# Performance work log

Measured on AMD Instinct MI355X. Metric: run time of the kernel, lower is better.

## Reference

```python
import jax, jax.numpy as jnp
import numpy as np
import math

D_POLY = 2  # polynomial order d
N_NODES = 50000
IN_FEATS = 128
H_FEATS = 64
N_EDGES = 800000


def calc_thetas(d):
    # Beta-wavelet polynomial coefficients (ascending order), matching calculate_theta2
    thetas = []
    for i in range(d + 1):
        p = np.poly1d([1.0])
        for _ in range(i):
            p = p * np.poly1d([0.5, 0.0])      # (x/2)
        for _ in range(d - i):
            p = p * np.poly1d([-0.5, 1.0])     # (1 - x/2)
        beta = math.gamma(i + 1) * math.gamma(d + 1 - i) / math.gamma(d + 2)
        p = p / beta
        asc = p.coeffs[::-1]                   # ascending coefficients
        asc = np.concatenate([asc, np.zeros(d + 1 - len(asc))])
        thetas.append(asc.astype(np.float32))
    return thetas

THETAS = calc_thetas(D_POLY)


def setup_inputs() -> dict:
    key = jax.random.key(0)
    ks = jax.random.split(key, 7)
    features = jax.random.normal(ks[0], (N_NODES, IN_FEATS), dtype=jnp.float32)
    src = jax.random.randint(ks[1], (N_EDGES,), 0, N_NODES)
    dst = jax.random.randint(ks[2], (N_EDGES,), 0, N_NODES)
    s1 = 1.0 / math.sqrt(IN_FEATS)
    W1 = jax.random.uniform(ks[3], (H_FEATS, IN_FEATS), jnp.float32, -s1, s1)
    b1 = jnp.zeros((H_FEATS,), jnp.float32)
    s2 = 1.0 / math.sqrt(H_FEATS * (D_POLY + 1))
    W2 = jax.random.uniform(ks[4], (H_FEATS, H_FEATS * (D_POLY + 1)), jnp.float32, -s2, s2)
    b2 = jnp.zeros((H_FEATS,), jnp.float32)
    return {"features": features, "src": src, "dst": dst,
            "W1": W1, "b1": b1, "W2": W2, "b2": b2}


def reference(features, src, dst, W1, b1, W2, b2):
    N = features.shape[0]
    # linear1 + ReLU
    x = jax.nn.relu(features @ W1.T + b1)  # [N, H]
    # D^{-1/2} from in-degrees (clamped at 1)
    deg = jax.ops.segment_sum(jnp.ones_like(dst, dtype=x.dtype), dst, num_segments=N)
    D_invsqrt = jnp.clip(deg, 1.0, None) ** -0.5  # [N]
    D_invsqrt = D_invsqrt[:, None]

    def unn_laplacian(f):
        # f - D^{-1/2} A D^{-1/2} f   (aggregation onto destination nodes)
        agg = jax.ops.segment_sum((f * D_invsqrt)[src], dst, num_segments=N)
        return f - agg * D_invsqrt

    outs = []
    for theta in THETAS:
        f = x
        h = theta[0] * x
        for k in range(1, len(theta)):
            f = unn_laplacian(f)
            h = h + theta[k] * f
        outs.append(h)
    feats_final = jnp.concatenate(outs, axis=-1)  # [N, H*(d+1)]
    return feats_final @ W2.T + b2
```

## Files before the change

### kernel.cpp

```cpp
#include <hip/hip_runtime.h>

#define NN 50000
#define NE 800000
#define INF 128
#define HF 64
#define K2 192
#define MAXDEG 64

typedef __attribute__((ext_vector_type(8))) short short8;
typedef __attribute__((ext_vector_type(4))) float float4v;
typedef __attribute__((ext_vector_type(4))) unsigned short ushort4v;
typedef __attribute__((ext_vector_type(2))) unsigned int uint2v;

__device__ inline unsigned short f2bf(float x) {
    unsigned int u = __float_as_uint(x);
    u += 0x7FFFu + ((u >> 16) & 1u);
    return (unsigned short)(u >> 16);
}
__device__ inline float bflo(unsigned int p) { return __uint_as_float(p << 16); }
__device__ inline float bfhi(unsigned int p) { return __uint_as_float(p & 0xFFFF0000u); }


__global__ __launch_bounds__(256) void fill_ell_part(const int* __restrict__ src,
                                                     const int* __restrict__ dst,
                                                     int* __restrict__ cnt,
                                                     unsigned short* __restrict__ ell) {
    int chunk = blockIdx.x >> 3;
    int p     = blockIdx.x & 7;
    int e = chunk * 256 + threadIdx.x;
    if (e >= NE) return;
    int d = dst[e];
    if (d / 6250 != p) return;
    int pos = atomicAdd(&cnt[d], 1);
    if (pos < MAXDEG) ell[d * MAXDEG + pos] = (unsigned short)src[e];
}

__global__ __launch_bounds__(256) void dinv_kernel(int* __restrict__ cnt,
                                                   float* __restrict__ dinv,
                                                   unsigned short* __restrict__ hb0,
                                                   unsigned short* __restrict__ hb1) {
    int i = blockIdx.x * 256 + threadIdx.x;
    if (i < NN) {
        int c = cnt[i];
        if (c > MAXDEG) c = MAXDEG;
        cnt[i] = c;
        dinv[i] = rsqrtf((float)(c < 1 ? 1 : c));
    }
    if (i < HF) {
        hb0[(size_t)NN * HF + i] = 0;
        hb1[(size_t)NN * HF + i] = 0;
    }
}


__global__ void pack_b(const float* __restrict__ W1, const float* __restrict__ W2,
                       unsigned short* __restrict__ Bp1, unsigned short* __restrict__ Bp2,
                       int* __restrict__ cnt) {
    int gid = blockIdx.x * 256 + threadIdx.x;
    for (int z = gid; z < NN; z += 20480) cnt[z] = 0;
    if (gid >= 20480) return;
    if (gid < 8192) {
        int j  = gid & 7;
        int l  = (gid >> 3) & 63;
        int nt = (gid >> 9) & 3;
        int kc = gid >> 11;
        int n = nt * 16 + (l & 15);
        int k = kc * 32 + (l >> 4) * 8 + j;
        Bp1[gid] = f2bf(W1[n * INF + k]);
    } else {
        int g = gid - 8192;
        int j  = g & 7;
        int l  = (g >> 3) & 63;
        int nt = (g >> 9) & 3;
        int kc = g >> 11;
        int n = nt * 16 + (l & 15);
        int k = kc * 32 + (l >> 4) * 8 + j;
        const float* row = W2 + (size_t)n * K2;
        float v;
        if (k < 64) {
            v = 3.0f * row[k];
        } else if (k < 128) {
            int c = k - 64;
            v = -3.0f * row[c] + 3.0f * row[64 + c];
        } else {
            int c = k - 128;
            v = 0.75f * row[c] - 1.5f * row[64 + c] + 0.75f * row[128 + c];
        }
        Bp2[g] = f2bf(v);
    }
}


__global__ __launch_bounds__(256) void gemm1_mfma(const float* __restrict__ F,
                                                  const unsigned short* __restrict__ Bp,
                                                  const float* __restrict__ b1,
                                                  const float* __restrict__ dinv,
                                                  unsigned short* __restrict__ xb,
                                                  unsigned short* __restrict__ hb0) {
    int tid  = threadIdx.x;
    int lane = tid & 63;
    int wv   = tid >> 6;
    int m0   = blockIdx.x * 64 + wv * 16;
    if (m0 >= NN) return;
    int mrow = lane & 15;
    int q    = lane >> 4;

    float4v acc[4];
#pragma unroll
    for (int nt = 0; nt < 4; ++nt) acc[nt] = (float4v){0.f, 0.f, 0.f, 0.f};

    const float* arow = F + (size_t)(m0 + mrow) * INF + q * 8;
#pragma unroll
    for (int kc = 0; kc < INF / 32; ++kc) {
        const float* ap = arow + kc * 32;
        float4v a0 = *reinterpret_cast<const float4v*>(ap);
        float4v a1 = *reinterpret_cast<const float4v*>(ap + 4);
        short8 af;
        af[0] = (short)f2bf(a0[0]); af[1] = (short)f2bf(a0[1]);
        af[2] = (short)f2bf(a0[2]); af[3] = (short)f2bf(a0[3]);
        af[4] = (short)f2bf(a1[0]); af[5] = (short)f2bf(a1[1]);
        af[6] = (short)f2bf(a1[2]); af[7] = (short)f2bf(a1[3]);
#pragma unroll
        for (int nt = 0; nt < 4; ++nt) {
            short8 bf = *reinterpret_cast<const short8*>(Bp + (((kc * 4 + nt) * 64 + lane) << 3));
            acc[nt] = __builtin_amdgcn_mfma_f32_16x16x32_bf16(af, bf, acc[nt], 0, 0, 0);
        }
    }

    float dn[4];
#pragma unroll
    for (int r = 0; r < 4; ++r) dn[r] = dinv[m0 + q * 4 + r];

#pragma unroll
    for (int nt = 0; nt < 4; ++nt) {
        int n = nt * 16 + mrow;
        float bv = b1[n];
#pragma unroll
        for (int r = 0; r < 4; ++r) {
            int node = m0 + q * 4 + r;
            float v = acc[nt][r] + bv;
            v = v > 0.0f ? v : 0.0f;
            xb [(size_t)node * HF + n] = f2bf(v);
            hb0[(size_t)node * HF + n] = f2bf(v * dn[r]);
        }
    }
}


template <bool WRITE_H>
__global__ __launch_bounds__(256) void gather_quad(const unsigned short* __restrict__ ell,
                                                   const int* __restrict__ cnt,
                                                   const float* __restrict__ dinv,
                                                   const unsigned short* __restrict__ fin,
                                                   const unsigned short* __restrict__ hb,
                                                   unsigned short* __restrict__ fout,
                                                   unsigned short* __restrict__ hout) {
    int lane  = threadIdx.x & 63;
    int wv    = threadIdx.x >> 6;
    int which = lane >> 4;
    int jj    = lane & 15;
    int n = blockIdx.x * 16 + wv * 4 + which;
    int deg = cnt[n];

    ushort4v ids = *reinterpret_cast<const ushort4v*>(ell + (size_t)n * MAXDEG + jj * 4);
    int slot = jj * 4;
    int s0 = (slot + 0 < deg) ? (int)ids[0] : NN;
    int s1 = (slot + 1 < deg) ? (int)ids[1] : NN;
    int s2 = (slot + 2 < deg) ? (int)ids[2] : NN;
    int s3 = (slot + 3 < deg) ? (int)ids[3] : NN;

    int wmax = deg;
    wmax = max(wmax, __shfl_xor(wmax, 16));
    wmax = max(wmax, __shfl_xor(wmax, 32));

    const uint2v* hbd = (const uint2v*)hb;
    int base = which * 16;

    float a0=0,a1=0,a2=0,a3=0;
    float b0=0,b1=0,b2=0,b3=0;
    float c0=0,c1=0,c2=0,c3=0;
    float d0=0,d1=0,d2=0,d3=0;

    for (int k = 0; k < wmax; k += 4) {
        int o = base + (k >> 2);
        int t0 = __shfl(s0, o), t1 = __shfl(s1, o);
        int t2 = __shfl(s2, o), t3 = __shfl(s3, o);
        uint2v p0 = hbd[(size_t)t0 * 16 + jj];
        uint2v p1 = hbd[(size_t)t1 * 16 + jj];
        uint2v p2 = hbd[(size_t)t2 * 16 + jj];
        uint2v p3 = hbd[(size_t)t3 * 16 + jj];
        a0 += bflo(p0[0]); a1 += bfhi(p0[0]); a2 += bflo(p0[1]); a3 += bfhi(p0[1]);
        b0 += bflo(p1[0]); b1 += bfhi(p1[0]); b2 += bflo(p1[1]); b3 += bfhi(p1[1]);
        c0 += bflo(p2[0]); c1 += bfhi(p2[0]); c2 += bflo(p2[1]); c3 += bfhi(p2[1]);
        d0 += bflo(p3[0]); d1 += bfhi(p3[0]); d2 += bflo(p3[1]); d3 += bfhi(p3[1]);
    }
    float e0 = (a0 + b0) + (c0 + d0);
    float e1 = (a1 + b1) + (c1 + d1);
    float e2 = (a2 + b2) + (c2 + d2);
    float e3 = (a3 + b3) + (c3 + d3);
    float dn = dinv[n];

    uint2v xv = ((const uint2v*)fin)[(size_t)n * 16 + jj];
    float f0 = bflo(xv[0]) - e0 * dn;
    float f1 = bfhi(xv[0]) - e1 * dn;
    float f2 = bflo(xv[1]) - e2 * dn;
    float f3 = bfhi(xv[1]) - e3 * dn;
    uint2v ov;
    ov[0] = (unsigned int)f2bf(f0) | ((unsigned int)f2bf(f1) << 16);
    ov[1] = (unsigned int)f2bf(f2) | ((unsigned int)f2bf(f3) << 16);
    ((uint2v*)fout)[(size_t)n * 16 + jj] = ov;
    if (WRITE_H) {
        uint2v hv;
        hv[0] = (unsigned int)f2bf(f0 * dn) | ((unsigned int)f2bf(f1 * dn) << 16);
        hv[1] = (unsigned int)f2bf(f2 * dn) | ((unsigned int)f2bf(f3 * dn) << 16);
        ((uint2v*)hout)[(size_t)n * 16 + jj] = hv;
    }
}


__global__ __launch_bounds__(256) void gemm2_mfma(const unsigned short* __restrict__ xb,
                                                  const unsigned short* __restrict__ f1b,
                                                  const unsigned short* __restrict__ f2b,
                                                  const unsigned short* __restrict__ Bp,
                                                  const float* __restrict__ b2,
                                                  float* __restrict__ out) {
    int tid  = threadIdx.x;
    int lane = tid & 63;
    int wv   = tid >> 6;
    int m0   = blockIdx.x * 64 + wv * 16;
    if (m0 >= NN) return;
    int mrow = lane & 15;
    int q    = lane >> 4;

    float4v acc[4];
#pragma unroll
    for (int nt = 0; nt < 4; ++nt) acc[nt] = (float4v){0.f, 0.f, 0.f, 0.f};

    const unsigned short* ax = xb  + (size_t)(m0 + mrow) * HF + q * 8;
    const unsigned short* a1 = f1b + (size_t)(m0 + mrow) * HF + q * 8;
    const unsigned short* a2 = f2b + (size_t)(m0 + mrow) * HF + q * 8;

#pragma unroll
    for (int kc = 0; kc < 6; ++kc) {
        short8 af;
        if (kc < 2)      af = *reinterpret_cast<const short8*>(ax + kc * 32);
        else if (kc < 4) af = *reinterpret_cast<const short8*>(a1 + (kc - 2) * 32);
        else             af = *reinterpret_cast<const short8*>(a2 + (kc - 4) * 32);
#pragma unroll
        for (int nt = 0; nt < 4; ++nt) {
            short8 bf = *reinterpret_cast<const short8*>(Bp + (((kc * 4 + nt) * 64 + lane) << 3));
            acc[nt] = __builtin_amdgcn_mfma_f32_16x16x32_bf16(af, bf, acc[nt], 0, 0, 0);
        }
    }

#pragma unroll
    for (int nt = 0; nt < 4; ++nt) {
        int n = nt * 16 + mrow;
        float bv = b2[n];
#pragma unroll
        for (int r = 0; r < 4; ++r) {
            int node = m0 + q * 4 + r;
            out[(size_t)node * HF + n] = acc[nt][r] + bv;
        }
    }
}


extern "C" void kernel_launch(void* const* d_in, const int* in_sizes, int n_in,
                              void* d_out, int out_size, void* d_ws, size_t ws_size,
                              hipStream_t stream) {
    const float* features = (const float*)d_in[0];
    const int*   src      = (const int*)d_in[1];
    const int*   dst      = (const int*)d_in[2];
    const float* W1       = (const float*)d_in[3];
    const float* b1       = (const float*)d_in[4];
    const float* W2       = (const float*)d_in[5];
    const float* b2       = (const float*)d_in[6];
    float* out = (float*)d_out;

    unsigned short* xb  = (unsigned short*)d_ws;
    unsigned short* hb0 = xb  + (size_t)NN * HF;
    unsigned short* f1b = hb0 + (size_t)(NN + 1) * HF;
    unsigned short* hb1 = f1b + (size_t)NN * HF;
    unsigned short* f2b = hb1 + (size_t)(NN + 1) * HF;
    unsigned short* Bp1 = f2b + (size_t)NN * HF;
    unsigned short* Bp2 = Bp1 + 8192;
    unsigned short* ell = Bp2 + 12288;
    int*   cnt  = (int*)(ell + (size_t)NN * MAXDEG);
    float* dinv = (float*)(cnt + NN);

    pack_b<<<80, 256, 0, stream>>>(W1, W2, Bp1, Bp2, cnt);

    fill_ell_part<<<((NE + 255) / 256) * 8, 256, 0, stream>>>(src, dst, cnt, ell);

    dinv_kernel<<<(NN + 255) / 256, 256, 0, stream>>>(cnt, dinv, hb0, hb1);

    gemm1_mfma<<<(NN + 63) / 64, 256, 0, stream>>>(features, Bp1, b1, dinv, xb, hb0);

    gather_quad<true ><<<NN / 16, 256, 0, stream>>>(ell, cnt, dinv, xb,  hb0, f1b, hb1);
    gather_quad<false><<<NN / 16, 256, 0, stream>>>(ell, cnt, dinv, f1b, hb1, f2b, nullptr);

    gemm2_mfma<<<(NN + 63) / 64, 256, 0, stream>>>(xb, f1b, f2b, Bp2, b2, out);
}
```

Baseline: 170.4 us.

## Fuse second gather into GEMM2, drop dinv kernel, vectorize ELL fill

Fuses the second Laplacian gather into the output GEMM. The f2 tile is staged in shared memory instead of being written to and re-read from global memory. The dinv kernel is removed: degree clamping and rsqrt are recomputed inline from cnt, and the sentinel-row zeroing moves into pack_b. The ELL fill now loads four dst entries per thread, and the gather loop is unrolled to issue two groups of loads per iteration. The cost is lower parallelism in the fused kernel (one wave handles 16 nodes sequentially) and extra LDS use.

```diff
diff --git a/kernel.cpp b/kernel.cpp
--- a/kernel.cpp
+++ b/kernel.cpp
@@ -27,37 +27,31 @@
                                                      unsigned short* __restrict__ ell) {
     int chunk = blockIdx.x >> 3;
     int p     = blockIdx.x & 7;
-    int e = chunk * 256 + threadIdx.x;
-    if (e >= NE) return;
-    int d = dst[e];
-    if (d / 6250 != p) return;
-    int pos = atomicAdd(&cnt[d], 1);
-    if (pos < MAXDEG) ell[d * MAXDEG + pos] = (unsigned short)src[e];
-}
-
-__global__ __launch_bounds__(256) void dinv_kernel(int* __restrict__ cnt,
-                                                   float* __restrict__ dinv,
-                                                   unsigned short* __restrict__ hb0,
-                                                   unsigned short* __restrict__ hb1) {
-    int i = blockIdx.x * 256 + threadIdx.x;
-    if (i < NN) {
-        int c = cnt[i];
-        if (c > MAXDEG) c = MAXDEG;
-        cnt[i] = c;
-        dinv[i] = rsqrtf((float)(c < 1 ? 1 : c));
-    }
-    if (i < HF) {
-        hb0[(size_t)NN * HF + i] = 0;
-        hb1[(size_t)NN * HF + i] = 0;
+    int e0 = (chunk * 256 + (int)threadIdx.x) * 4;
+    if (e0 >= NE) return;
+    int4 d4 = *reinterpret_cast<const int4*>(dst + e0);
+    int dd[4] = {d4.x, d4.y, d4.z, d4.w};
+#pragma unroll
+    for (int j = 0; j < 4; ++j) {
+        int d = dd[j];
+        if (d / 6250 == p) {
+            int pos = atomicAdd(&cnt[d], 1);
+            if (pos < MAXDEG) ell[d * MAXDEG + pos] = (unsigned short)src[e0 + j];
+        }
     }
 }
 
 
 __global__ void pack_b(const float* __restrict__ W1, const float* __restrict__ W2,
                        unsigned short* __restrict__ Bp1, unsigned short* __restrict__ Bp2,
-                       int* __restrict__ cnt) {
+                       int* __restrict__ cnt,
+                       unsigned short* __restrict__ hb0, unsigned short* __restrict__ hb1) {
     int gid = blockIdx.x * 256 + threadIdx.x;
     for (int z = gid; z < NN; z += 20480) cnt[z] = 0;
+    if (gid < HF) {
+        hb0[(size_t)NN * HF + gid] = 0;
+        hb1[(size_t)NN * HF + gid] = 0;
+    }
     if (gid >= 20480) return;
     if (gid < 8192) {
         int j  = gid & 7;
@@ -94,7 +88,7 @@
 __global__ __launch_bounds__(256) void gemm1_mfma(const float* __restrict__ F,
                                                   const unsigned short* __restrict__ Bp,
                                                   const float* __restrict__ b1,
-                                                  const float* __restrict__ dinv,
+                                                  const int* __restrict__ cnt,
                                                   unsigned short* __restrict__ xb,
                                                   unsigned short* __restrict__ hb0) {
     int tid  = threadIdx.x;
@@ -129,7 +123,11 @@
 
     float dn[4];
 #pragma unroll
-    for (int r = 0; r < 4; ++r) dn[r] = dinv[m0 + q * 4 + r];
+    for (int r = 0; r < 4; ++r) {
+        int c = cnt[m0 + q * 4 + r];
+        c = c > MAXDEG ? MAXDEG : c;
+        dn[r] = rsqrtf((float)(c < 1 ? 1 : c));
+    }
 
 #pragma unroll
     for (int nt = 0; nt < 4; ++nt) {
@@ -147,10 +145,48 @@
 }
 
 
-template <bool WRITE_H>
+__device__ inline void gather_accum(const uint2v* __restrict__ hbd,
+                                    int s0, int s1, int s2, int s3,
+                                    int wmax, int base, int jj,
+                                    float& e0, float& e1, float& e2, float& e3) {
+    float a0=0,a1=0,a2=0,a3=0;
+    float b0=0,b1=0,b2=0,b3=0;
+    float c0=0,c1=0,c2=0,c3=0;
+    float d0=0,d1=0,d2=0,d3=0;
+    for (int k = 0; k < wmax; k += 8) {
+        int o = base + (k >> 2);
+        int t0 = __shfl(s0, o), t1 = __shfl(s1, o);
+        int t2 = __shfl(s2, o), t3 = __shfl(s3, o);
+        uint2v p0 = hbd[(size_t)t0 * 16 + jj];
+        uint2v p1 = hbd[(size_t)t1 * 16 + jj];
+        uint2v p2 = hbd[(size_t)t2 * 16 + jj];
+        uint2v p3 = hbd[(size_t)t3 * 16 + jj];
+        if (k + 4 < wmax) {
+            int u0 = __shfl(s0, o + 1), u1 = __shfl(s1, o + 1);
+            int u2 = __shfl(s2, o + 1), u3 = __shfl(s3, o + 1);
+            uint2v q0 = hbd[(size_t)u0 * 16 + jj];
+            uint2v q1 = hbd[(size_t)u1 * 16 + jj];
+            uint2v q2 = hbd[(size_t)u2 * 16 + jj];
+            uint2v q3 = hbd[(size_t)u3 * 16 + jj];
+            a0 += bflo(q0[0]); a1 += bfhi(q0[0]); a2 += bflo(q0[1]); a3 += bfhi(q0[1]);
+            b0 += bflo(q1[0]); b1 += bfhi(q1[0]); b2 += bflo(q1[1]); b3 += bfhi(q1[1]);
+            c0 += bflo(q2[0]); c1 += bfhi(q2[0]); c2 += bflo(q2[1]); c3 += bfhi(q2[1]);
+            d0 += bflo(q3[0]); d1 += bfhi(q3[0]); d2 += bflo(q3[1]); d3 += bfhi(q3[1]);
+        }
+        a0 += bflo(p0[0]); a1 += bfhi(p0[0]); a2 += bflo(p0[1]); a3 += bfhi(p0[1]);
+        b0 += bflo(p1[0]); b1 += bfhi(p1[0]); b2 += bflo(p1[1]); b3 += bfhi(p1[1]);
+        c0 += bflo(p2[0]); c1 += bfhi(p2[0]); c2 += bflo(p2[1]); c3 += bfhi(p2[1]);
+        d0 += bflo(p3[0]); d1 += bfhi(p3[0]); d2 += bflo(p3[1]); d3 += bfhi(p3[1]);
+    }
+    e0 = (a0 + b0) + (c0 + d0);
+    e1 = (a1 + b1) + (c1 + d1);
+    e2 = (a2 + b2) + (c2 + d2);
+    e3 = (a3 + b3) + (c3 + d3);
+}
+
+
 __global__ __launch_bounds__(256) void gather_quad(const unsigned short* __restrict__ ell,
                                                    const int* __restrict__ cnt,
-                                                   const float* __restrict__ dinv,
                                                    const unsigned short* __restrict__ fin,
                                                    const unsigned short* __restrict__ hb,
                                                    unsigned short* __restrict__ fout,
@@ -161,6 +197,7 @@
     int jj    = lane & 15;
     int n = blockIdx.x * 16 + wv * 4 + which;
     int deg = cnt[n];
+    deg = deg > MAXDEG ? MAXDEG : deg;
 
     ushort4v ids = *reinterpret_cast<const ushort4v*>(ell + (size_t)n * MAXDEG + jj * 4);
     int slot = jj * 4;
@@ -173,32 +210,10 @@
     wmax = max(wmax, __shfl_xor(wmax, 16));
     wmax = max(wmax, __shfl_xor(wmax, 32));
 
-    const uint2v* hbd = (const uint2v*)hb;
-    int base = which * 16;
-
-    float a0=0,a1=0,a2=0,a3=0;
-    float b0=0,b1=0,b2=0,b3=0;
-    float c0=0,c1=0,c2=0,c3=0;
-    float d0=0,d1=0,d2=0,d3=0;
-
-    for (int k = 0; k < wmax; k += 4) {
-        int o = base + (k >> 2);
-        int t0 = __shfl(s0, o), t1 = __shfl(s1, o);
-        int t2 = __shfl(s2, o), t3 = __shfl(s3, o);
-        uint2v p0 = hbd[(size_t)t0 * 16 + jj];
-        uint2v p1 = hbd[(size_t)t1 * 16 + jj];
-        uint2v p2 = hbd[(size_t)t2 * 16 + jj];
-        uint2v p3 = hbd[(size_t)t3 * 16 + jj];
-        a0 += bflo(p0[0]); a1 += bfhi(p0[0]); a2 += bflo(p0[1]); a3 += bfhi(p0[1]);
-        b0 += bflo(p1[0]); b1 += bfhi(p1[0]); b2 += bflo(p1[1]); b3 += bfhi(p1[1]);
-        c0 += bflo(p2[0]); c1 += bfhi(p2[0]); c2 += bflo(p2[1]); c3 += bfhi(p2[1]);
-        d0 += bflo(p3[0]); d1 += bfhi(p3[0]); d2 += bflo(p3[1]); d3 += bfhi(p3[1]);
-    }
-    float e0 = (a0 + b0) + (c0 + d0);
-    float e1 = (a1 + b1) + (c1 + d1);
-    float e2 = (a2 + b2) + (c2 + d2);
-    float e3 = (a3 + b3) + (c3 + d3);
-    float dn = dinv[n];
+    float e0, e1, e2, e3;
+    gather_accum((const uint2v*)hb, s0, s1, s2, s3, wmax, which * 16, jj, e0, e1, e2, e3);
+
+    float dn = rsqrtf((float)(deg < 1 ? 1 : deg));
 
     uint2v xv = ((const uint2v*)fin)[(size_t)n * 16 + jj];
     float f0 = bflo(xv[0]) - e0 * dn;
@@ -209,43 +224,77 @@
     ov[0] = (unsigned int)f2bf(f0) | ((unsigned int)f2bf(f1) << 16);
     ov[1] = (unsigned int)f2bf(f2) | ((unsigned int)f2bf(f3) << 16);
     ((uint2v*)fout)[(size_t)n * 16 + jj] = ov;
-    if (WRITE_H) {
-        uint2v hv;
-        hv[0] = (unsigned int)f2bf(f0 * dn) | ((unsigned int)f2bf(f1 * dn) << 16);
-        hv[1] = (unsigned int)f2bf(f2 * dn) | ((unsigned int)f2bf(f3 * dn) << 16);
-        ((uint2v*)hout)[(size_t)n * 16 + jj] = hv;
-    }
-}
-
-
-__global__ __launch_bounds__(256) void gemm2_mfma(const unsigned short* __restrict__ xb,
-                                                  const unsigned short* __restrict__ f1b,
-                                                  const unsigned short* __restrict__ f2b,
-                                                  const unsigned short* __restrict__ Bp,
-                                                  const float* __restrict__ b2,
-                                                  float* __restrict__ out) {
+    uint2v hv;
+    hv[0] = (unsigned int)f2bf(f0 * dn) | ((unsigned int)f2bf(f1 * dn) << 16);
+    hv[1] = (unsigned int)f2bf(f2 * dn) | ((unsigned int)f2bf(f3 * dn) << 16);
+    ((uint2v*)hout)[(size_t)n * 16 + jj] = hv;
+}
+
+
+__global__ __launch_bounds__(256) void gather_gemm2(const unsigned short* __restrict__ ell,
+                                                    const int* __restrict__ cnt,
+                                                    const unsigned short* __restrict__ xb,
+                                                    const unsigned short* __restrict__ f1b,
+                                                    const unsigned short* __restrict__ hb1,
+                                                    const unsigned short* __restrict__ Bp,
+                                                    const float* __restrict__ b2,
+                                                    float* __restrict__ out) {
+    __shared__ __align__(16) unsigned int f2l[4][16 * 68];
     int tid  = threadIdx.x;
     int lane = tid & 63;
     int wv   = tid >> 6;
-    int m0   = blockIdx.x * 64 + wv * 16;
-    if (m0 >= NN) return;
+    int nb   = blockIdx.x * 64 + wv * 16;
+    if (nb >= NN) return;
+    unsigned int* myl = f2l[wv];
+
+    int which = lane >> 4;
+    int jj    = lane & 15;
+    const uint2v* hbd = (const uint2v*)hb1;
+
+#pragma unroll
+    for (int q = 0; q < 4; ++q) {
+        int n = nb + q * 4 + which;
+        int deg = cnt[n];
+        deg = deg > MAXDEG ? MAXDEG : deg;
+        ushort4v ids = *reinterpret_cast<const ushort4v*>(ell + (size_t)n * MAXDEG + jj * 4);
+        int slot = jj * 4;
+        int s0 = (slot + 0 < deg) ? (int)ids[0] : NN;
+        int s1 = (slot + 1 < deg) ? (int)ids[1] : NN;
+        int s2 = (slot + 2 < deg) ? (int)ids[2] : NN;
+        int s3 = (slot + 3 < deg) ? (int)ids[3] : NN;
+        int wmax = deg;
+        wmax = max(wmax, __shfl_xor(wmax, 16));
+        wmax = max(wmax, __shfl_xor(wmax, 32));
+
+        float e0, e1, e2, e3;
+        gather_accum(hbd, s0, s1, s2, s3, wmax, which * 16, jj, e0, e1, e2, e3);
+
+        float dn = rsqrtf((float)(deg < 1 ? 1 : deg));
+        uint2v xv = ((const uint2v*)f1b)[(size_t)n * 16 + jj];
+        float f0 = bflo(xv[0]) - e0 * dn;
+        float f1 = bfhi(xv[0]) - e1 * dn;
+        float f2 = bflo(xv[1]) - e2 * dn;
+        float f3 = bfhi(xv[1]) - e3 * dn;
+        int row = q * 4 + which;
+        myl[row * 68 + jj * 2]     = (unsigned int)f2bf(f0) | ((unsigned int)f2bf(f1) << 16);
+        myl[row * 68 + jj * 2 + 1] = (unsigned int)f2bf(f2) | ((unsigned int)f2bf(f3) << 16);
+    }
+
     int mrow = lane & 15;
-    int q    = lane >> 4;
-
+    int qq   = lane >> 4;
     float4v acc[4];
 #pragma unroll
     for (int nt = 0; nt < 4; ++nt) acc[nt] = (float4v){0.f, 0.f, 0.f, 0.f};
 
-    const unsigned short* ax = xb  + (size_t)(m0 + mrow) * HF + q * 8;
-    const unsigned short* a1 = f1b + (size_t)(m0 + mrow) * HF + q * 8;
-    const unsigned short* a2 = f2b + (size_t)(m0 + mrow) * HF + q * 8;
+    const unsigned short* ax  = xb  + (size_t)(nb + mrow) * HF + qq * 8;
+    const unsigned short* a1p = f1b + (size_t)(nb + mrow) * HF + qq * 8;
 
 #pragma unroll
     for (int kc = 0; kc < 6; ++kc) {
         short8 af;
         if (kc < 2)      af = *reinterpret_cast<const short8*>(ax + kc * 32);
-        else if (kc < 4) af = *reinterpret_cast<const short8*>(a1 + (kc - 2) * 32);
-        else             af = *reinterpret_cast<const short8*>(a2 + (kc - 4) * 32);
+        else if (kc < 4) af = *reinterpret_cast<const short8*>(a1p + (kc - 2) * 32);
+        else             af = *reinterpret_cast<const short8*>(myl + mrow * 68 + (kc - 4) * 16 + qq * 4);
 #pragma unroll
         for (int nt = 0; nt < 4; ++nt) {
             short8 bf = *reinterpret_cast<const short8*>(Bp + (((kc * 4 + nt) * 64 + lane) << 3));
@@ -255,12 +304,12 @@
 
 #pragma unroll
     for (int nt = 0; nt < 4; ++nt) {
-        int n = nt * 16 + mrow;
-        float bv = b2[n];
+        int n2 = nt * 16 + mrow;
+        float bv = b2[n2];
 #pragma unroll
         for (int r = 0; r < 4; ++r) {
-            int node = m0 + q * 4 + r;
-            out[(size_t)node * HF + n] = acc[nt][r] + bv;
+            int node = nb + qq * 4 + r;
+            out[(size_t)node * HF + n2] = acc[nt][r] + bv;
         }
     }
 }
@@ -282,23 +331,18 @@
     unsigned short* hb0 = xb  + (size_t)NN * HF;
     unsigned short* f1b = hb0 + (size_t)(NN + 1) * HF;
     unsigned short* hb1 = f1b + (size_t)NN * HF;
-    unsigned short* f2b = hb1 + (size_t)(NN + 1) * HF;
-    unsigned short* Bp1 = f2b + (size_t)NN * HF;
+    unsigned short* Bp1 = hb1 + (size_t)(NN + 1) * HF;
     unsigned short* Bp2 = Bp1 + 8192;
     unsigned short* ell = Bp2 + 12288;
     int*   cnt  = (int*)(ell + (size_t)NN * MAXDEG);
-    float* dinv = (float*)(cnt + NN);
-
-    pack_b<<<80, 256, 0, stream>>>(W1, W2, Bp1, Bp2, cnt);
-
-    fill_ell_part<<<((NE + 255) / 256) * 8, 256, 0, stream>>>(src, dst, cnt, ell);
-
-    dinv_kernel<<<(NN + 255) / 256, 256, 0, stream>>>(cnt, dinv, hb0, hb1);
-
-    gemm1_mfma<<<(NN + 63) / 64, 256, 0, stream>>>(features, Bp1, b1, dinv, xb, hb0);
-
-    gather_quad<true ><<<NN / 16, 256, 0, stream>>>(ell, cnt, dinv, xb,  hb0, f1b, hb1);
-    gather_quad<false><<<NN / 16, 256, 0, stream>>>(ell, cnt, dinv, f1b, hb1, f2b, nullptr);
-
-    gemm2_mfma<<<(NN + 63) / 64, 256, 0, stream>>>(xb, f1b, f2b, Bp2, b2, out);
-}
+
+    pack_b<<<80, 256, 0, stream>>>(W1, W2, Bp1, Bp2, cnt, hb0, hb1);
+
+    fill_ell_part<<<((NE + 1023) / 1024) * 8, 256, 0, stream>>>(src, dst, cnt, ell);
+
+    gemm1_mfma<<<(NN + 63) / 64, 256, 0, stream>>>(features, Bp1, b1, cnt, xb, hb0);
+
+    gather_quad<<<NN / 16, 256, 0, stream>>>(ell, cnt, xb, hb0, f1b, hb1);
+
+    gather_gemm2<<<(NN + 63) / 64, 256, 0, stream>>>(ell, cnt, xb, f1b, hb1, Bp2, b2, out);
+}
```

After: 170.5 us. About the same (+0.1%).
